# Kernel tuning notes

Measured on AMD Instinct MI355X. Metric: run time of the kernel, lower is better.

Reference implementation:

```python
import jax, jax.numpy as jnp
import numpy as np

EMBED_DIM = 1024
NUM_HEADS = 16
HEAD_DIM = EMBED_DIM // NUM_HEADS
SCALE = HEAD_DIM ** -0.5
B, S = 2, 2048


def setup_inputs() -> dict:
    key = jax.random.key(0)
    ks = jax.random.split(key, 11)
    lim = 1.0 / np.sqrt(EMBED_DIM)
    def lin(kw, kb):
        W = jax.random.uniform(kw, (EMBED_DIM, EMBED_DIM), jnp.float32, -lim, lim)
        b = jax.random.uniform(kb, (EMBED_DIM,), jnp.float32, -lim, lim)
        return W, b
    Wq, bq = lin(ks[0], ks[1])
    Wk, bk = lin(ks[2], ks[3])
    Wv, bv = lin(ks[4], ks[5])
    Wo, bo = lin(ks[6], ks[7])
    query = jax.random.normal(ks[8], (B, S, EMBED_DIM), jnp.float32)
    key_t = jax.random.normal(ks[9], (B, S, EMBED_DIM), jnp.float32)
    value = jax.random.normal(ks[10], (B, S, EMBED_DIM), jnp.float32)
    return {"query": query, "key": key_t, "value": value,
            "Wq": Wq, "bq": bq, "Wk": Wk, "bk": bk,
            "Wv": Wv, "bv": bv, "Wo": Wo, "bo": bo}


def reference(query, key, value, Wq, bq, Wk, bk, Wv, bv, Wo, bo):
    # 'flash' path with attn_mask=None == full softmax attention (chunking is
    # only an execution schedule; per-chunk softmax is over the full key axis).
    b, s, _ = query.shape
    def heads(x, W, bias):
        y = x @ W.T + bias                      # [b, s, E]
        return y.reshape(b, s, NUM_HEADS, HEAD_DIM).transpose(0, 2, 1, 3)  # [b, h, s, d]
    q = heads(query, Wq, bq)
    k = heads(key, Wk, bk)
    v = heads(value, Wv, bv)
    scores = jnp.einsum('bhqd,bhkd->bhqk', q, k) * SCALE
    attn = jax.nn.softmax(scores, axis=-1)
    out = jnp.einsum('bhqk,bhkd->bhqd', attn, v)
    out = out.transpose(0, 2, 1, 3).reshape(b, s, EMBED_DIM)
    return out @ Wo.T + bo
```

## Files before the change

### kernel.cpp

```cpp
#include <hip/hip_runtime.h>

typedef unsigned short u16;
typedef unsigned int u32;
typedef __attribute__((ext_vector_type(8))) __bf16 bf16x8;
typedef __attribute__((ext_vector_type(4))) float f32x4;
typedef __attribute__((ext_vector_type(16))) float f32x16;
typedef __attribute__((ext_vector_type(4))) unsigned short u16x4;
typedef __attribute__((ext_vector_type(8))) unsigned short u16x8;
typedef __attribute__((ext_vector_type(4))) unsigned int u32x4;

#define DEV static __device__ __forceinline__

DEV void async_copy16(const void* g, void* l) {
  __builtin_amdgcn_global_load_lds((const __attribute__((address_space(1))) void*)g,
                                   (__attribute__((address_space(3))) void*)l, 16, 0, 0);
}
DEV float b2f(u16 s) { union { unsigned u; float f; } v; v.u = ((unsigned)s) << 16; return v.f; }
DEV u16 f2b(float f) {
  union { float f; unsigned u; } v; v.f = f;
  unsigned r = v.u + 0x7FFFu + ((v.u >> 16) & 1u);
  return (u16)(r >> 16);
}
DEV u32 pack2bf(float a, float b) {
  u32 ua = __float_as_uint(a) + 0x8000u;
  u32 ub = __float_as_uint(b) + 0x8000u;
  return __builtin_amdgcn_perm(ub, ua, 0x07060302u);
}
DEV int wave_detect_bf16(const unsigned* q, int lane) {
  const unsigned w = q[lane & 63];
  const unsigned e = (w >> 7) & 0xFFu;
  const bool inr = (e >= 100u && e <= 132u);
  return (__popcll(__ballot(inr)) >= 48) ? 1 : 0;
}

#define MFMA(a, b, c) __builtin_amdgcn_mfma_f32_16x16x32_bf16((a), (b), (c), 0, 0, 0)
#define MFMA32(a, b, c) __builtin_amdgcn_mfma_f32_32x32x16_bf16((a), (b), (c), 0, 0, 0)

__global__ void convert_inputs(
    const void* s0, const void* s1, const void* s2,
    const void* s3, const void* s4, const void* s5, const void* s6,
    const void* s7, const void* s8, const void* s9, const void* s10,
    u16* __restrict__ d0, u16* __restrict__ d1, u16* __restrict__ d2,
    u16* __restrict__ d3, u16* __restrict__ d4, u16* __restrict__ d5, u16* __restrict__ d6,
    float* __restrict__ e7, float* __restrict__ e8, float* __restrict__ e9, float* __restrict__ e10)
{
  const int bi = blockIdx.y;
  const void* src = nullptr; u16* db = nullptr; float* df = nullptr; int n = 0;
  switch (bi) {
    case 0:  src = s0;  db = d0; n = 4194304; break;
    case 1:  src = s1;  db = d1; n = 4194304; break;
    case 2:  src = s2;  db = d2; n = 4194304; break;
    case 3:  src = s3;  db = d3; n = 1048576; break;
    case 4:  src = s4;  db = d4; n = 1048576; break;
    case 5:  src = s5;  db = d5; n = 1048576; break;
    case 6:  src = s6;  db = d6; n = 1048576; break;
    case 7:  src = s7;  df = e7; n = 1024; break;
    case 8:  src = s8;  df = e8; n = 1024; break;
    case 9:  src = s9;  df = e9; n = 1024; break;
    default: src = s10; df = e10; n = 1024; break;
  }
  const int isbf = wave_detect_bf16((const unsigned*)s0, threadIdx.x);
  const int stride = gridDim.x * 256 * 8;
  for (int i = (blockIdx.x * 256 + threadIdx.x) * 8; i < n; i += stride) {
    if (db) {
      u16x8 v;
      if (isbf) {
        v = *(const u16x8*)((const u16*)src + i);
      } else {
        const f32x4* sf = (const f32x4*)((const float*)src + i);
        const f32x4 x0 = sf[0], x1 = sf[1];
#pragma unroll
        for (int j = 0; j < 4; ++j) { v[j] = f2b(x0[j]); v[4 + j] = f2b(x1[j]); }
      }
      *(u16x8*)(db + i) = v;
    } else {
#pragma unroll
      for (int j = 0; j < 8; ++j) {
        float x = isbf ? b2f(((const u16*)src)[i + j]) : ((const float*)src)[i + j];
        df[i + j] = x;
      }
    }
  }
}

__global__ __launch_bounds__(256, 3)
void gemm_qkv(const u16* __restrict__ X0, const u16* __restrict__ X1, const u16* __restrict__ X2,
              const u16* __restrict__ W0, const u16* __restrict__ W1, const u16* __restrict__ W2,
              const float* __restrict__ B0, const float* __restrict__ B1, const float* __restrict__ B2,
              u16* __restrict__ Y0, u16* __restrict__ Y1, u16* __restrict__ Y2,
              float* __restrict__ Yf, const unsigned* __restrict__ qdet, int mode0)
{
  __shared__ __align__(16) u16 smem[17408];
  u16* As = smem;
  u16* Bs = smem + 8192;

  const int z = blockIdx.z;
  const u16* X  = (z == 0) ? X0 : ((z == 1) ? X1 : X2);
  const u16* W  = (z == 0) ? W0 : ((z == 1) ? W1 : W2);
  const float* Bi = (z == 0) ? B0 : ((z == 1) ? B1 : B2);
  u16* Y        = (z == 0) ? Y0 : ((z == 1) ? Y1 : Y2);
  const int mode = mode0 ? mode0 : z;

  const int t = threadIdx.x, wave = t >> 6, lane = t & 63;
  const int lane15 = lane & 15, quad = lane >> 4, l7 = lane15 & 7;
  const int m0 = blockIdx.y * 128, n0 = blockIdx.x * 128;

  const int srow = lane >> 3;
  const int schunk = (lane & 7) ^ srow;
  const u16* gA = X + (size_t)(m0 + wave * 32 + srow) * 1024 + schunk * 8;
  const u16* gB = W + (size_t)(n0 + wave * 32 + srow) * 1024 + schunk * 8;
  u16* lA = &As[wave * 32 * 64];
  u16* lB = &Bs[wave * 32 * 64];

  f32x4 acc[4][4];
#pragma unroll
  for (int i = 0; i < 4; ++i)
#pragma unroll
    for (int j = 0; j < 4; ++j) acc[i][j] = (f32x4){0.f, 0.f, 0.f, 0.f};

  const int wr = wave >> 1, wc = wave & 1;

  for (int k0 = 0; k0 < 1024; k0 += 64) {
#pragma unroll
    for (int r = 0; r < 4; ++r) async_copy16(gA + (size_t)r * 8 * 1024, lA + r * 8 * 64);
#pragma unroll
    for (int r = 0; r < 4; ++r) async_copy16(gB + (size_t)r * 8 * 1024, lB + r * 8 * 64);
    gA += 64; gB += 64;
    __syncthreads();

#pragma unroll
    for (int kk = 0; kk < 2; ++kk) {
      bf16x8 af[4], bfv[4];
#pragma unroll
      for (int mt = 0; mt < 4; ++mt)
        af[mt] = *(const bf16x8*)&As[(wr * 64 + mt * 16 + lane15) * 64 + ((kk * 4 + quad) ^ l7) * 8];
#pragma unroll
      for (int nt = 0; nt < 4; ++nt)
        bfv[nt] = *(const bf16x8*)&Bs[(wc * 64 + nt * 16 + lane15) * 64 + ((kk * 4 + quad) ^ l7) * 8];
#pragma unroll
      for (int mt = 0; mt < 4; ++mt)
#pragma unroll
        for (int nt = 0; nt < 4; ++nt)
          acc[mt][nt] = MFMA(af[mt], bfv[nt], acc[mt][nt]);
    }
    __syncthreads();
  }

  const float qscale = 0.125f * 1.44269504088896340736f;

  if (mode == 2) {
    u16* T2 = smem;
    __syncthreads();
#pragma unroll
    for (int mt = 0; mt < 4; ++mt) {
      const int sl_base = wr * 64 + mt * 16 + quad * 4;
#pragma unroll
      for (int nt = 0; nt < 4; ++nt) {
        const int nn = wc * 64 + nt * 16 + lane15;
        const float bias_v = Bi[n0 + nn];
#pragma unroll
        for (int r = 0; r < 4; ++r)
          T2[nn * 136 + sl_base + r] = f2b(acc[mt][nt][r] + bias_v);
      }
    }
    __syncthreads();
    const size_t grow0 = (size_t)(m0 >> 11) * 1024 + n0;
    const int col0 = m0 & 2047;
#pragma unroll
    for (int i = 0; i < 8; ++i) {
      const int id = i * 256 + t;
      const int row = id >> 4, ch = id & 15;
      *(u16x8*)&Y[(grow0 + row) * 2048 + col0 + ch * 8] = *(const u16x8*)&T2[row * 136 + ch * 8];
    }
    return;
  }

  const int outbf = (mode == 3) ? wave_detect_bf16(qdet, lane) : 1;

#pragma unroll
  for (int mt = 0; mt < 4; ++mt) {
    const int m_base = m0 + wr * 64 + mt * 16 + quad * 4;
#pragma unroll
    for (int nt = 0; nt < 4; ++nt) {
      const int n = n0 + wc * 64 + nt * 16 + lane15;
      const float bias_v = Bi[n];
#pragma unroll
      for (int r = 0; r < 4; ++r) {
        const int m = m_base + r;
        float v = acc[mt][nt][r] + bias_v;
        if (mode == 0) v *= qscale;
        if (mode == 3) {
          if (outbf) Y[(size_t)m * 1024 + n] = f2b(v);
          else       Yf[(size_t)m * 1024 + n] = v;
        } else {
          size_t addr = (((size_t)(m >> 11) * 16 + (n >> 6)) * 2048 + (size_t)(m & 2047)) * 64 + (n & 63);
          Y[addr] = f2b(v);
        }
      }
    }
  }
}

__global__ __launch_bounds__(256, 2)
void flash_attn(const u16* __restrict__ Qs, const u16* __restrict__ Ks,
                const u16* __restrict__ Vt, u16* __restrict__ AO)
{
  __shared__ __align__(16) u16 smem[16384];
  u16* Kt = smem;
  u16* Vs = smem + 8192;

  const int t = threadIdx.x, w = t >> 6, lane = t & 63;
  const int l31 = lane & 31, half = lane >> 5;
  const int bh = blockIdx.y;
  const int q0 = blockIdx.x * 128;

  const u16* Qb = Qs + ((size_t)bh * 2048 + q0) * 64;
  const u16* Kb = Ks + (size_t)bh * 2048 * 64;
  const u16* Vb = Vt + (size_t)bh * 64 * 2048;

  const int krow = lane >> 3;
  const int kchunk = (lane & 7) ^ krow;
  const int vrow = lane >> 4;
  const int vcb = lane & 15;

#pragma unroll
  for (int r = 0; r < 4; ++r)
    async_copy16(Qb + (size_t)(r * 32 + w * 8 + krow) * 64 + kchunk * 8,
                 &Kt[(r * 32 + w * 8) * 64]);
  __syncthreads();
  const int qrow = w * 32 + l31;
  bf16x8 bq[4];
#pragma unroll
  for (int ks = 0; ks < 4; ++ks)
    bq[ks] = *(const bf16x8*)&Kt[qrow * 64 + (((ks * 2 + half) ^ (qrow & 7))) * 8];
  __syncthreads();

  f32x16 acc[2];
#pragma unroll
  for (int dt = 0; dt < 2; ++dt)
#pragma unroll
    for (int i = 0; i < 16; ++i) acc[dt][i] = 0.f;
  float lpart = 0.f;

  for (int kt = 0; kt < 16; ++kt) {
#pragma unroll
    for (int r = 0; r < 4; ++r)
      async_copy16(Kb + (size_t)(kt * 128 + r * 32 + w * 8 + krow) * 64 + kchunk * 8,
                   &Kt[(r * 32 + w * 8) * 64]);
#pragma unroll
    for (int r = 0; r < 4; ++r) {
      const int d = r * 16 + w * 4 + vrow;
      async_copy16(Vb + (size_t)d * 2048 + kt * 128 + (vcb ^ (d & 7)) * 8,
                   &Vs[(r * 16 + w * 4) * 128]);
    }
    __syncthreads();

#pragma unroll
    for (int ktile = 0; ktile < 4; ++ktile) {
      const int key = ktile * 32 + l31;
      f32x16 st;
#pragma unroll
      for (int i = 0; i < 16; ++i) st[i] = 0.f;
#pragma unroll
      for (int ks = 0; ks < 4; ++ks) {
        const bf16x8 ak = *(const bf16x8*)&Kt[key * 64 + (((ks * 2 + half) ^ (key & 7))) * 8];
        st = MFMA32(ak, bq[ks], st);
      }
      float p[16];
      float ts = 0.f;
#pragma unroll
      for (int i = 0; i < 16; ++i) { p[i] = __builtin_amdgcn_exp2f(st[i]); ts += p[i]; }
      lpart += ts;
      u32 pk0[4], pk1[4];
#pragma unroll
      for (int rq = 0; rq < 4; ++rq) {
        pk0[rq] = pack2bf(p[4 * rq + 0], p[4 * rq + 1]);
        pk1[rq] = pack2bf(p[4 * rq + 2], p[4 * rq + 3]);
      }
#pragma unroll
      for (int s2 = 0; s2 < 2; ++s2) {
        const u32 own0 = half ? pk0[2 * s2 + 1] : pk0[2 * s2];
        const u32 own1 = half ? pk1[2 * s2 + 1] : pk1[2 * s2];
        const u32 snd0 = half ? pk0[2 * s2] : pk0[2 * s2 + 1];
        const u32 snd1 = half ? pk1[2 * s2] : pk1[2 * s2 + 1];
        const u32 rcv0 = (u32)__shfl_xor((int)snd0, 32);
        const u32 rcv1 = (u32)__shfl_xor((int)snd1, 32);
        u32x4 bp;
        bp[0] = half ? rcv0 : own0;
        bp[1] = half ? rcv1 : own1;
        bp[2] = half ? own0 : rcv0;
        bp[3] = half ? own1 : rcv1;
        const bf16x8 bfrag = __builtin_bit_cast(bf16x8, bp);
#pragma unroll
        for (int dt = 0; dt < 2; ++dt) {
          const int d = dt * 32 + l31;
          const int c = ktile * 4 + s2 * 2 + half;
          const bf16x8 av = *(const bf16x8*)&Vs[d * 128 + ((c ^ (d & 7))) * 8];
          acc[dt] = MFMA32(av, bfrag, acc[dt]);
        }
      }
    }
    __syncthreads();
  }

  const float lfull = lpart + __shfl_xor(lpart, 32);
  const float rl = 1.0f / lfull;

  u16* T = smem;
#pragma unroll
  for (int dt = 0; dt < 2; ++dt)
#pragma unroll
    for (int rq = 0; rq < 4; ++rq) {
      u16x4 v4;
#pragma unroll
      for (int o = 0; o < 4; ++o) v4[o] = f2b(acc[dt][rq * 4 + o] * rl);
      *(u16x4*)&T[qrow * 72 + dt * 32 + rq * 8 + half * 4] = v4;
    }
  __syncthreads();

  const int b = bh >> 4, h = bh & 15;
#pragma unroll
  for (int i = 0; i < 4; ++i) {
    const int id = i * 256 + t;
    const int row = id >> 3, ch = id & 7;
    *(u16x8*)&AO[((size_t)b * 2048 + q0 + row) * 1024 + h * 64 + ch * 8] =
        *(const u16x8*)&T[row * 72 + ch * 8];
  }
}

extern "C" void kernel_launch(void* const* d_in, const int* in_sizes, int n_in,
                              void* d_out, int out_size, void* d_ws, size_t ws_size,
                              hipStream_t stream)
{
  const void* query = d_in[0];
  const void* key_  = d_in[1];
  const void* value = d_in[2];
  const void* Wq = d_in[3]; const void* bq = d_in[4];
  const void* Wk = d_in[5]; const void* bk = d_in[6];
  const void* Wv = d_in[7]; const void* bv = d_in[8];
  const void* Wo = d_in[9]; const void* bo = d_in[10];

  u16* ws = (u16*)d_ws;
  u16* Qs  = ws;
  u16* Ks  = Qs + 4194304;
  u16* Vt  = Ks + 4194304;
  u16* AO  = Vt + 4194304;
  u16* Xq  = AO + 4194304;
  u16* Xk  = Xq + 4194304;
  u16* Xv  = Xk + 4194304;
  u16* Wqc = Xv + 4194304;
  u16* Wkc = Wqc + 1048576;
  u16* Wvc = Wkc + 1048576;
  u16* Woc = Wvc + 1048576;
  float* Bc = (float*)(Woc + 1048576);

  convert_inputs<<<dim3(128, 11), 256, 0, stream>>>(
      query, key_, value, Wq, Wk, Wv, Wo, bq, bk, bv, bo,
      Xq, Xk, Xv, Wqc, Wkc, Wvc, Woc,
      Bc, Bc + 1024, Bc + 2048, Bc + 3072);

  gemm_qkv<<<dim3(8, 32, 3), 256, 0, stream>>>(Xq, Xk, Xv, Wqc, Wkc, Wvc,
                                               Bc, Bc + 1024, Bc + 2048,
                                               Qs, Ks, Vt, nullptr,
                                               (const unsigned*)query, 0);
  flash_attn<<<dim3(16, 32), 256, 0, stream>>>(Qs, Ks, Vt, AO);
  gemm_qkv<<<dim3(8, 32, 1), 256, 0, stream>>>(AO, AO, AO, Woc, Woc, Woc,
                                               Bc + 3072, Bc + 3072, Bc + 3072,
                                               (u16*)d_out, (u16*)d_out, (u16*)d_out,
                                               (float*)d_out, (const unsigned*)query, 3);
}
```

Baseline: 232.0 us.

## Double-buffer K/V tiles in flash attention and stage projection stores via LDS

The flash attention kernel now uses two LDS buffers so the next K/V tile's async loads are issued before computing on the current tile, hiding global load latency behind the MFMA work. The kernel also remaps the block index so that blocks sharing a query tile across heads run adjacently, which may improve L2 reuse. Separately, the projection epilogues now stage bf16 results in shared memory and write them out as coalesced 16-byte vector stores instead of scattered 2-byte stores. LDS use in the attention kernel doubles to 64 KB, which may limit occupancy.

```diff
diff --git a/kernel.cpp b/kernel.cpp
--- a/kernel.cpp
+++ b/kernel.cpp
@@ -175,29 +175,72 @@
     return;
   }
 
-  const int outbf = (mode == 3) ? wave_detect_bf16(qdet, lane) : 1;
-
+  if (mode == 3) {
+    const int outbf = wave_detect_bf16(qdet, lane);
+    if (outbf) {
+      u16* T2 = smem;
+      __syncthreads();
+#pragma unroll
+      for (int mt = 0; mt < 4; ++mt) {
+        const int ml = wr * 64 + mt * 16 + quad * 4;
+#pragma unroll
+        for (int nt = 0; nt < 4; ++nt) {
+          const int nl = wc * 64 + nt * 16 + lane15;
+          const float bias_v = Bi[n0 + nl];
+#pragma unroll
+          for (int r = 0; r < 4; ++r)
+            T2[(ml + r) * 136 + nl] = f2b(acc[mt][nt][r] + bias_v);
+        }
+      }
+      __syncthreads();
+#pragma unroll
+      for (int i = 0; i < 8; ++i) {
+        const int id = i * 256 + t;
+        const int row = id >> 4, ch = id & 15;
+        *(u16x8*)&Y[(size_t)(m0 + row) * 1024 + n0 + ch * 8] = *(const u16x8*)&T2[row * 136 + ch * 8];
+      }
+    } else {
+#pragma unroll
+      for (int mt = 0; mt < 4; ++mt) {
+        const int m_base = m0 + wr * 64 + mt * 16 + quad * 4;
+#pragma unroll
+        for (int nt = 0; nt < 4; ++nt) {
+          const int n = n0 + wc * 64 + nt * 16 + lane15;
+          const float bias_v = Bi[n];
+#pragma unroll
+          for (int r = 0; r < 4; ++r)
+            Yf[(size_t)(m_base + r) * 1024 + n] = acc[mt][nt][r] + bias_v;
+        }
+      }
+    }
+    return;
+  }
+
+  u16* T3 = smem;
+  __syncthreads();
 #pragma unroll
   for (int mt = 0; mt < 4; ++mt) {
-    const int m_base = m0 + wr * 64 + mt * 16 + quad * 4;
+    const int sl = wr * 64 + mt * 16 + quad * 4;
 #pragma unroll
     for (int nt = 0; nt < 4; ++nt) {
-      const int n = n0 + wc * 64 + nt * 16 + lane15;
-      const float bias_v = Bi[n];
+      const int d_loc = nt * 16 + lane15;
+      const float bias_v = Bi[n0 + wc * 64 + d_loc];
 #pragma unroll
       for (int r = 0; r < 4; ++r) {
-        const int m = m_base + r;
         float v = acc[mt][nt][r] + bias_v;
         if (mode == 0) v *= qscale;
-        if (mode == 3) {
-          if (outbf) Y[(size_t)m * 1024 + n] = f2b(v);
-          else       Yf[(size_t)m * 1024 + n] = v;
-        } else {
-          size_t addr = (((size_t)(m >> 11) * 16 + (n >> 6)) * 2048 + (size_t)(m & 2047)) * 64 + (n & 63);
-          Y[addr] = f2b(v);
-        }
-      }
-    }
+        T3[wc * 8704 + (sl + r) * 68 + d_loc] = f2b(v);
+      }
+    }
+  }
+  __syncthreads();
+  const int bb = m0 >> 11, s0 = m0 & 2047, h0 = n0 >> 6;
+#pragma unroll
+  for (int i = 0; i < 8; ++i) {
+    const int id = i * 256 + t;
+    const int hh = id >> 10, row = (id >> 3) & 127, ch = id & 7;
+    *(u16x8*)&Y[(((size_t)bb * 16 + h0 + hh) * 2048 + s0 + row) * 64 + ch * 8] =
+        *(const u16x8*)&T3[hh * 8704 + row * 68 + ch * 8];
   }
 }
 
@@ -205,14 +248,13 @@
 void flash_attn(const u16* __restrict__ Qs, const u16* __restrict__ Ks,
                 const u16* __restrict__ Vt, u16* __restrict__ AO)
 {
-  __shared__ __align__(16) u16 smem[16384];
-  u16* Kt = smem;
-  u16* Vs = smem + 8192;
+  __shared__ __align__(16) u16 smem[32768];
 
   const int t = threadIdx.x, w = t >> 6, lane = t & 63;
   const int l31 = lane & 31, half = lane >> 5;
-  const int bh = blockIdx.y;
-  const int q0 = blockIdx.x * 128;
+  const int lin = blockIdx.y * 16 + blockIdx.x;
+  const int bh = lin & 31;
+  const int q0 = (lin >> 5) * 128;
 
   const u16* Qb = Qs + ((size_t)bh * 2048 + q0) * 64;
   const u16* Kb = Ks + (size_t)bh * 2048 * 64;
@@ -226,13 +268,28 @@
 #pragma unroll
   for (int r = 0; r < 4; ++r)
     async_copy16(Qb + (size_t)(r * 32 + w * 8 + krow) * 64 + kchunk * 8,
-                 &Kt[(r * 32 + w * 8) * 64]);
+                 &smem[(r * 32 + w * 8) * 64]);
   __syncthreads();
   const int qrow = w * 32 + l31;
   bf16x8 bq[4];
 #pragma unroll
   for (int ks = 0; ks < 4; ++ks)
-    bq[ks] = *(const bf16x8*)&Kt[qrow * 64 + (((ks * 2 + half) ^ (qrow & 7))) * 8];
+    bq[ks] = *(const bf16x8*)&smem[qrow * 64 + (((ks * 2 + half) ^ (qrow & 7))) * 8];
+
+  {
+    u16* Kn = smem + 16384;
+    u16* Vn = smem + 24576;
+#pragma unroll
+    for (int r = 0; r < 4; ++r)
+      async_copy16(Kb + (size_t)(r * 32 + w * 8 + krow) * 64 + kchunk * 8,
+                   &Kn[(r * 32 + w * 8) * 64]);
+#pragma unroll
+    for (int r = 0; r < 4; ++r) {
+      const int d = r * 16 + w * 4 + vrow;
+      async_copy16(Vb + (size_t)d * 2048 + (vcb ^ (d & 7)) * 8,
+                   &Vn[(r * 16 + w * 4) * 128]);
+    }
+  }
   __syncthreads();
 
   f32x16 acc[2];
@@ -243,17 +300,22 @@
   float lpart = 0.f;
 
   for (int kt = 0; kt < 16; ++kt) {
-#pragma unroll
-    for (int r = 0; r < 4; ++r)
-      async_copy16(Kb + (size_t)(kt * 128 + r * 32 + w * 8 + krow) * 64 + kchunk * 8,
-                   &Kt[(r * 32 + w * 8) * 64]);
-#pragma unroll
-    for (int r = 0; r < 4; ++r) {
-      const int d = r * 16 + w * 4 + vrow;
-      async_copy16(Vb + (size_t)d * 2048 + kt * 128 + (vcb ^ (d & 7)) * 8,
-                   &Vs[(r * 16 + w * 4) * 128]);
-    }
-    __syncthreads();
+    u16* Kc = smem + ((kt + 1) & 1) * 16384;
+    u16* Vc = Kc + 8192;
+    if (kt < 15) {
+      u16* Kn = smem + (kt & 1) * 16384;
+      u16* Vn = Kn + 8192;
+#pragma unroll
+      for (int r = 0; r < 4; ++r)
+        async_copy16(Kb + (size_t)((kt + 1) * 128 + r * 32 + w * 8 + krow) * 64 + kchunk * 8,
+                     &Kn[(r * 32 + w * 8) * 64]);
+#pragma unroll
+      for (int r = 0; r < 4; ++r) {
+        const int d = r * 16 + w * 4 + vrow;
+        async_copy16(Vb + (size_t)d * 2048 + (kt + 1) * 128 + (vcb ^ (d & 7)) * 8,
+                     &Vn[(r * 16 + w * 4) * 128]);
+      }
+    }
 
 #pragma unroll
     for (int ktile = 0; ktile < 4; ++ktile) {
@@ -263,7 +325,7 @@
       for (int i = 0; i < 16; ++i) st[i] = 0.f;
 #pragma unroll
       for (int ks = 0; ks < 4; ++ks) {
-        const bf16x8 ak = *(const bf16x8*)&Kt[key * 64 + (((ks * 2 + half) ^ (key & 7))) * 8];
+        const bf16x8 ak = *(const bf16x8*)&Kc[key * 64 + (((ks * 2 + half) ^ (key & 7))) * 8];
         st = MFMA32(ak, bq[ks], st);
       }
       float p[16];
@@ -295,7 +357,7 @@
         for (int dt = 0; dt < 2; ++dt) {
           const int d = dt * 32 + l31;
           const int c = ktile * 4 + s2 * 2 + half;
-          const bf16x8 av = *(const bf16x8*)&Vs[d * 128 + ((c ^ (d & 7))) * 8];
+          const bf16x8 av = *(const bf16x8*)&Vc[d * 128 + ((c ^ (d & 7))) * 8];
           acc[dt] = MFMA32(av, bfrag, acc[dt]);
         }
       }
```

New measurement: 233.9 us. No clear change (+0.8%).
